# Optimization experiments

Measured on AMD Instinct MI355X. Metric: run time of the kernel, lower is better.

The kernel has to match this reference:

```python
import jax, jax.numpy as jnp
import numpy as np

HEADS = 8
DIM_HEAD = 64
SCALE = DIM_HEAD ** -0.5

def setup_inputs() -> dict:
    key = jax.random.key(0)
    ks = jax.random.split(key, 6)
    b, n, m, qd, cd = 4, 2048, 2048, 256, 256
    inner = HEADS * DIM_HEAD
    return {
        "x": jax.random.normal(ks[0], (b, n, qd), jnp.float32),
        "context": jax.random.normal(ks[1], (b, m, cd), jnp.float32),
        "Wq": jax.random.normal(ks[2], (inner, qd), jnp.float32) * 0.02,
        "bq": jnp.zeros((inner,), jnp.float32),
        "Wkv": jax.random.normal(ks[3], (2 * inner, cd), jnp.float32) * 0.02,
        "bkv": jnp.zeros((2 * inner,), jnp.float32),
        "Wo": jax.random.normal(ks[4], (qd, inner), jnp.float32) * 0.02,
        "bo": jnp.zeros((qd,), jnp.float32),
    }

def reference(x, context, Wq, bq, Wkv, bkv, Wo, bo):
    b, n, _ = x.shape
    m = context.shape[1]
    inner = HEADS * DIM_HEAD
    # 1x1 conv projections == pointwise linear
    q = jnp.einsum('bnd,ed->bne', x, Wq) + bq            # [b, n, inner]
    kv = jnp.einsum('bmd,ed->bme', context, Wkv) + bkv    # [b, m, 2*inner]
    k, v = kv[..., :inner], kv[..., inner:]
    q = q.reshape(b, n, HEADS, DIM_HEAD).transpose(0, 2, 1, 3)  # [b,h,n,d]
    k = k.reshape(b, m, HEADS, DIM_HEAD).transpose(0, 2, 1, 3)
    v = v.reshape(b, m, HEADS, DIM_HEAD).transpose(0, 2, 1, 3)
    sim = jnp.einsum('bhid,bhjd->bhij', q, k) * SCALE     # [b,h,n,m]
    attn = jax.nn.softmax(sim, axis=-1)
    out = jnp.einsum('bhij,bhjd->bhid', attn, v)          # [b,h,n,d]
    out = out.transpose(0, 2, 1, 3).reshape(b, n, inner)  # [b,n,inner]
    return jnp.einsum('bne,oe->bno', out, Wo) + bo        # [b,n,query_dim]
```

## Files before the change

### kernel.cpp

```cpp
#include <hip/hip_runtime.h>
#include <hip/hip_bf16.h>

#define NB 4
#define SEQ 2048
#define NHEADS 8

typedef __attribute__((ext_vector_type(8))) short bf16x8;
typedef __attribute__((ext_vector_type(4))) short bf16x4;
typedef __attribute__((ext_vector_type(4))) float f32x4;

__device__ inline short f2bf(float x) {
    union { float f; unsigned u; } v; v.f = x;
    unsigned r = v.u + 0x7FFF + ((v.u >> 16) & 1);
    return (short)(r >> 16);
}

__device__ inline unsigned pack2bf(float a, float b) {
    __hip_bfloat162 h = __float22bfloat162_rn(make_float2(a, b));
    unsigned u; __builtin_memcpy(&u, &h, 4);
    return u;
}

__global__ __launch_bounds__(256) void cvt_all(
    const float* __restrict__ x, const float* __restrict__ ctx,
    const float* __restrict__ wq, const float* __restrict__ wkv,
    const float* __restrict__ wo,
    short* __restrict__ xb, short* __restrict__ cb, short* __restrict__ wqb,
    short* __restrict__ wkvb, short* __restrict__ wob)
{
    const int i = blockIdx.x * 256 + threadIdx.x;
    const float* src; short* dst; int off;
    if (i < 524288)       { src = x;   dst = xb;   off = i; }
    else if (i < 1048576) { src = ctx; dst = cb;   off = i - 524288; }
    else if (i < 1081344) { src = wq;  dst = wqb;  off = i - 1048576; }
    else if (i < 1146880) { src = wkv; dst = wkvb; off = i - 1081344; }
    else                  { src = wo;  dst = wob;  off = i - 1146880; }
    const float4 v = ((const float4*)src)[off];
    uint2 o2;
    o2.x = pack2bf(v.x, v.y);
    o2.y = pack2bf(v.z, v.w);
    *(uint2*)(dst + (size_t)off * 4) = o2;
}

template <bool OUT_BF16>
__global__ __launch_bounds__(256) void gemm_bf16(
    const short* __restrict__ A,
    const short* __restrict__ W,
    const float* __restrict__ bias,
    void* __restrict__ out,
    int K, int Ccols, float scale)
{
    __shared__ short As[128 * 64];
    __shared__ short Ws[128 * 64];
    const int tid = threadIdx.x;
    const int w = tid >> 6;
    const int lane = tid & 63;
    const int low = lane & 15;
    const int quad = lane >> 4;
    const int wm = w >> 1;
    const int wn = w & 1;
    const int rM0 = blockIdx.y * 128;
    const int c0 = blockIdx.x * 128;

    const int srow = tid >> 3;
    const int sj = tid & 7;

    f32x4 acc[4][4];
#pragma unroll
    for (int mt = 0; mt < 4; ++mt)
#pragma unroll
        for (int nt = 0; nt < 4; ++nt) acc[mt][nt] = (f32x4){0.f, 0.f, 0.f, 0.f};

    bf16x8 pa[4], pwr[4];
#pragma unroll
    for (int c = 0; c < 4; ++c) {
        const int row = c * 32 + srow;
        pa[c]  = *(const bf16x8*)(A + (size_t)(rM0 + row) * K + sj * 8);
        pwr[c] = *(const bf16x8*)(W + (size_t)(c0 + row) * K + sj * 8);
    }

    int k0 = 0;
    for (;;) {
        __syncthreads();
#pragma unroll
        for (int c = 0; c < 4; ++c) {
            const int row = c * 32 + srow;
            const int pc = sj ^ (row & 7);
            *(bf16x8*)(&As[row * 64 + pc * 8]) = pa[c];
            *(bf16x8*)(&Ws[row * 64 + pc * 8]) = pwr[c];
        }
        __syncthreads();
        const int kn = k0 + 64;
        if (kn < K) {
#pragma unroll
            for (int c = 0; c < 4; ++c) {
                const int row = c * 32 + srow;
                pa[c]  = *(const bf16x8*)(A + (size_t)(rM0 + row) * K + kn + sj * 8);
                pwr[c] = *(const bf16x8*)(W + (size_t)(c0 + row) * K + kn + sj * 8);
            }
        }
#pragma unroll
        for (int kh = 0; kh < 2; ++kh) {
            bf16x8 af[4], bfv[4];
#pragma unroll
            for (int t = 0; t < 4; ++t) {
                const int ra = wm * 64 + t * 16 + low;
                af[t] = *(const bf16x8*)(&As[ra * 64 + ((kh * 4 + quad) ^ (ra & 7)) * 8]);
                const int rb = wn * 64 + t * 16 + low;
                bfv[t] = *(const bf16x8*)(&Ws[rb * 64 + ((kh * 4 + quad) ^ (rb & 7)) * 8]);
            }
#pragma unroll
            for (int mt = 0; mt < 4; ++mt)
#pragma unroll
                for (int nt = 0; nt < 4; ++nt)
                    acc[mt][nt] = __builtin_amdgcn_mfma_f32_16x16x32_bf16(af[mt], bfv[nt], acc[mt][nt], 0, 0, 0);
        }
        k0 = kn;
        if (k0 >= K) break;
    }

#pragma unroll
    for (int nt = 0; nt < 4; ++nt) {
        const int col = c0 + wn * 64 + nt * 16 + low;
        const float bv = bias[col];
#pragma unroll
        for (int mt = 0; mt < 4; ++mt) {
            const size_t rbase = (size_t)(rM0 + wm * 64 + mt * 16 + quad * 4);
#pragma unroll
            for (int r = 0; r < 4; ++r) {
                const float val = (acc[mt][nt][r] + bv) * scale;
                if (OUT_BF16) ((short*)out)[(rbase + r) * Ccols + col] = f2bf(val);
                else          ((float*)out)[(rbase + r) * Ccols + col] = val;
            }
        }
    }
}

#define KST 72
#define VST 72
#define PST 72

__global__ __launch_bounds__(256) void attn_mfma(
    const short* __restrict__ q2,
    const short* __restrict__ kv2,
    short* __restrict__ o)
{
    __shared__ short Ks[64 * KST];
    __shared__ short Vt[64 * VST];
    __shared__ short Ps[4][32 * PST];

    const int tid = threadIdx.x;
    const int w = tid >> 6;
    const int lane = tid & 63;
    const int low = lane & 15;
    const int quad = lane >> 4;

    const int bh = blockIdx.y;
    const int b = bh >> 3;
    const int h = bh & 7;
    const int iq0 = blockIdx.x * 128;

    bf16x8 qf[2][2];
#pragma unroll
    for (int qt = 0; qt < 2; ++qt)
#pragma unroll
        for (int kh = 0; kh < 2; ++kh)
            qf[qt][kh] = *(const bf16x8*)(q2 + (size_t)(b * SEQ + iq0 + w * 32 + qt * 16 + low) * 512
                                          + h * 64 + kh * 32 + quad * 8);

    const short* kbase = kv2 + (size_t)(b * SEQ) * 1024 + h * 64;
    const short* vbase = kbase + 512;
    short* pw = &Ps[w][0];

    float lsum[2][4];
#pragma unroll
    for (int qt = 0; qt < 2; ++qt)
#pragma unroll
        for (int r = 0; r < 4; ++r) lsum[qt][r] = 0.f;
    f32x4 oacc[2][4];
#pragma unroll
    for (int qt = 0; qt < 2; ++qt)
#pragma unroll
        for (int dt = 0; dt < 4; ++dt) oacc[qt][dt] = (f32x4){0.f, 0.f, 0.f, 0.f};

    const int krow = tid >> 2;
    const int kc = (tid & 3) * 16;
    const int vk4 = (tid & 15) * 4;
    const int vd4 = (tid >> 4) * 4;

    bf16x8 pk0, pk1;
    bf16x4 pv0, pv1, pv2, pv3;
    {
        const short* ksrc = kbase + (size_t)krow * 1024 + kc;
        pk0 = *(const bf16x8*)(ksrc);
        pk1 = *(const bf16x8*)(ksrc + 8);
        const short* vs = vbase + (size_t)vk4 * 1024 + vd4;
        pv0 = *(const bf16x4*)(vs);
        pv1 = *(const bf16x4*)(vs + 1024);
        pv2 = *(const bf16x4*)(vs + 2048);
        pv3 = *(const bf16x4*)(vs + 3072);
    }

    for (int jt = 0; jt < SEQ / 64; ++jt) {
        __syncthreads();
        *(bf16x8*)(&Ks[krow * KST + kc]) = pk0;
        *(bf16x8*)(&Ks[krow * KST + kc + 8]) = pk1;
        {
            bf16x4 c0_, c1_, c2_, c3_;
            c0_[0] = pv0[0]; c0_[1] = pv1[0]; c0_[2] = pv2[0]; c0_[3] = pv3[0];
            c1_[0] = pv0[1]; c1_[1] = pv1[1]; c1_[2] = pv2[1]; c1_[3] = pv3[1];
            c2_[0] = pv0[2]; c2_[1] = pv1[2]; c2_[2] = pv2[2]; c2_[3] = pv3[2];
            c3_[0] = pv0[3]; c3_[1] = pv1[3]; c3_[2] = pv2[3]; c3_[3] = pv3[3];
            *(bf16x4*)(&Vt[(vd4 + 0) * VST + vk4]) = c0_;
            *(bf16x4*)(&Vt[(vd4 + 1) * VST + vk4]) = c1_;
            *(bf16x4*)(&Vt[(vd4 + 2) * VST + vk4]) = c2_;
            *(bf16x4*)(&Vt[(vd4 + 3) * VST + vk4]) = c3_;
        }
        __syncthreads();

        if (jt + 1 < SEQ / 64) {
            const short* ksrc = kbase + (size_t)((jt + 1) * 64 + krow) * 1024 + kc;
            pk0 = *(const bf16x8*)(ksrc);
            pk1 = *(const bf16x8*)(ksrc + 8);
            const short* vs = vbase + (size_t)((jt + 1) * 64 + vk4) * 1024 + vd4;
            pv0 = *(const bf16x4*)(vs);
            pv1 = *(const bf16x4*)(vs + 1024);
            pv2 = *(const bf16x4*)(vs + 2048);
            pv3 = *(const bf16x4*)(vs + 3072);
        }

#pragma unroll
        for (int nt = 0; nt < 4; ++nt) {
            const bf16x8 kb0 = *(const bf16x8*)(&Ks[(nt * 16 + low) * KST + quad * 8]);
            const bf16x8 kb1 = *(const bf16x8*)(&Ks[(nt * 16 + low) * KST + 32 + quad * 8]);
#pragma unroll
            for (int qt = 0; qt < 2; ++qt) {
                f32x4 s = (f32x4){0.f, 0.f, 0.f, 0.f};
                s = __builtin_amdgcn_mfma_f32_16x16x32_bf16(qf[qt][0], kb0, s, 0, 0, 0);
                s = __builtin_amdgcn_mfma_f32_16x16x32_bf16(qf[qt][1], kb1, s, 0, 0, 0);
                const float p0 = __builtin_amdgcn_exp2f(s[0]);
                const float p1 = __builtin_amdgcn_exp2f(s[1]);
                const float p2 = __builtin_amdgcn_exp2f(s[2]);
                const float p3 = __builtin_amdgcn_exp2f(s[3]);
                lsum[qt][0] += p0; lsum[qt][1] += p1;
                lsum[qt][2] += p2; lsum[qt][3] += p3;
                const unsigned u01 = pack2bf(p0, p1);
                const unsigned u23 = pack2bf(p2, p3);
                short* pb = &pw[(qt * 16 + quad * 4) * PST + nt * 16 + low];
                pb[0]       = (short)(u01 & 0xffff);
                pb[PST]     = (short)(u01 >> 16);
                pb[2 * PST] = (short)(u23 & 0xffff);
                pb[3 * PST] = (short)(u23 >> 16);
            }
        }
        __builtin_amdgcn_wave_barrier();

#pragma unroll
        for (int kb = 0; kb < 2; ++kb) {
            bf16x8 pfr[2];
#pragma unroll
            for (int qt = 0; qt < 2; ++qt)
                pfr[qt] = *(const bf16x8*)(&pw[(qt * 16 + low) * PST + kb * 32 + quad * 8]);
#pragma unroll
            for (int dt = 0; dt < 4; ++dt) {
                const bf16x8 vf = *(const bf16x8*)(&Vt[(dt * 16 + low) * VST + kb * 32 + quad * 8]);
                oacc[0][dt] = __builtin_amdgcn_mfma_f32_16x16x32_bf16(pfr[0], vf, oacc[0][dt], 0, 0, 0);
                oacc[1][dt] = __builtin_amdgcn_mfma_f32_16x16x32_bf16(pfr[1], vf, oacc[1][dt], 0, 0, 0);
            }
        }
        __builtin_amdgcn_wave_barrier();
    }

#pragma unroll
    for (int qt = 0; qt < 2; ++qt) {
        float linv[4];
#pragma unroll
        for (int r = 0; r < 4; ++r) {
            float x = lsum[qt][r];
            x += __shfl_xor(x, 1);
            x += __shfl_xor(x, 2);
            x += __shfl_xor(x, 4);
            x += __shfl_xor(x, 8);
            linv[r] = 1.f / x;
        }
        short* obase = o + (size_t)(b * SEQ + iq0 + w * 32 + qt * 16 + quad * 4) * 512 + h * 64;
#pragma unroll
        for (int r = 0; r < 4; ++r)
#pragma unroll
            for (int dt = 0; dt < 4; ++dt)
                obase[(size_t)r * 512 + dt * 16 + low] = f2bf(oacc[qt][dt][r] * linv[r]);
    }
}

extern "C" void kernel_launch(void* const* d_in, const int* in_sizes, int n_in,
                              void* d_out, int out_size, void* d_ws, size_t ws_size,
                              hipStream_t stream) {
    const float* x   = (const float*)d_in[0];
    const float* ctx = (const float*)d_in[1];
    const float* Wq  = (const float*)d_in[2];
    const float* bq  = (const float*)d_in[3];
    const float* Wkv = (const float*)d_in[4];
    const float* bkv = (const float*)d_in[5];
    const float* Wo  = (const float*)d_in[6];
    const float* bo  = (const float*)d_in[7];
    float* out = (float*)d_out;

    const int ROWS = NB * SEQ;
    short* xb   = (short*)d_ws;
    short* cb   = xb + 2097152;
    short* wqb  = cb + 2097152;
    short* wkvb = wqb + 131072;
    short* wob  = wkvb + 262144;
    short* q2b  = wob + 131072;
    short* kv2b = q2b + (size_t)ROWS * 512;
    short* owsb = kv2b + (size_t)ROWS * 1024;

    cvt_all<<<4608, 256, 0, stream>>>(x, ctx, Wq, Wkv, Wo, xb, cb, wqb, wkvb, wob);

    const float qscale = 0.125f * 1.44269504088896f;
    gemm_bf16<true><<<dim3(512 / 128, ROWS / 128), 256, 0, stream>>>(
        xb, wqb, bq, q2b, 256, 512, qscale);
    gemm_bf16<true><<<dim3(1024 / 128, ROWS / 128), 256, 0, stream>>>(
        cb, wkvb, bkv, kv2b, 256, 1024, 1.0f);
    attn_mfma<<<dim3(SEQ / 128, NB * NHEADS), 256, 0, stream>>>(q2b, kv2b, owsb);
    gemm_bf16<false><<<dim3(256 / 128, ROWS / 128), 256, 0, stream>>>(
        owsb, wob, bo, out, 512, 256, 1.0f);
}
```

Measured before the change: 170.1 us.

## Fuse fp32-to-bf16 conversion into GEMMs, shrink tiles, restructure attention per wave

The separate conversion kernel is removed, and each GEMM now loads fp32 inputs and weights and packs them to bf16 while staging into shared memory. This saves one launch and a full round trip of converted activations through global memory. The Q and output projections switch to a 64x64 tile variant to get more blocks. The attention kernel now gives each wave 16 query rows instead of 32, doubling the grid, and computes S transposed (K as the A operand) so P can be written with vector stores. The trade-offs are less K/V reuse per block in attention and twice the fp32 bytes loaded in the GEMMs.

```diff
diff --git a/kernel.cpp b/kernel.cpp
--- a/kernel.cpp
+++ b/kernel.cpp
@@ -21,49 +21,28 @@
     return u;
 }
 
-__global__ __launch_bounds__(256) void cvt_all(
-    const float* __restrict__ x, const float* __restrict__ ctx,
-    const float* __restrict__ wq, const float* __restrict__ wkv,
-    const float* __restrict__ wo,
-    short* __restrict__ xb, short* __restrict__ cb, short* __restrict__ wqb,
-    short* __restrict__ wkvb, short* __restrict__ wob)
-{
-    const int i = blockIdx.x * 256 + threadIdx.x;
-    const float* src; short* dst; int off;
-    if (i < 524288)       { src = x;   dst = xb;   off = i; }
-    else if (i < 1048576) { src = ctx; dst = cb;   off = i - 524288; }
-    else if (i < 1081344) { src = wq;  dst = wqb;  off = i - 1048576; }
-    else if (i < 1146880) { src = wkv; dst = wkvb; off = i - 1081344; }
-    else                  { src = wo;  dst = wob;  off = i - 1146880; }
-    const float4 v = ((const float4*)src)[off];
-    uint2 o2;
-    o2.x = pack2bf(v.x, v.y);
-    o2.y = pack2bf(v.z, v.w);
-    *(uint2*)(dst + (size_t)off * 4) = o2;
-}
-
-template <bool OUT_BF16>
-__global__ __launch_bounds__(256) void gemm_bf16(
-    const short* __restrict__ A,
-    const short* __restrict__ W,
-    const float* __restrict__ bias,
-    void* __restrict__ out,
+__device__ inline bf16x8 pack8(float4 a, float4 b) {
+    union { unsigned u[4]; bf16x8 v; } r;
+    r.u[0] = pack2bf(a.x, a.y);
+    r.u[1] = pack2bf(a.z, a.w);
+    r.u[2] = pack2bf(b.x, b.y);
+    r.u[3] = pack2bf(b.z, b.w);
+    return r.v;
+}
+
+template <bool CVT_A, bool CVT_W, bool OUT_BF16>
+__global__ __launch_bounds__(256) void gemm128(
+    const void* __restrict__ A_, const void* __restrict__ W_,
+    const float* __restrict__ bias, void* __restrict__ out,
     int K, int Ccols, float scale)
 {
     __shared__ short As[128 * 64];
     __shared__ short Ws[128 * 64];
     const int tid = threadIdx.x;
-    const int w = tid >> 6;
-    const int lane = tid & 63;
-    const int low = lane & 15;
-    const int quad = lane >> 4;
-    const int wm = w >> 1;
-    const int wn = w & 1;
-    const int rM0 = blockIdx.y * 128;
-    const int c0 = blockIdx.x * 128;
-
-    const int srow = tid >> 3;
-    const int sj = tid & 7;
+    const int w = tid >> 6, lane = tid & 63, low = lane & 15, quad = lane >> 4;
+    const int wm = w >> 1, wn = w & 1;
+    const int rM0 = blockIdx.y * 128, c0 = blockIdx.x * 128;
+    const int srow = tid >> 3, sj = tid & 7;
 
     f32x4 acc[4][4];
 #pragma unroll
@@ -71,13 +50,32 @@
 #pragma unroll
         for (int nt = 0; nt < 4; ++nt) acc[mt][nt] = (f32x4){0.f, 0.f, 0.f, 0.f};
 
-    bf16x8 pa[4], pwr[4];
-#pragma unroll
-    for (int c = 0; c < 4; ++c) {
+    float4 paf[4][2], pwf[4][2];
+    bf16x8 pab[4], pwb[4];
+
+    auto loadA = [&](int c, int k0) {
         const int row = c * 32 + srow;
-        pa[c]  = *(const bf16x8*)(A + (size_t)(rM0 + row) * K + sj * 8);
-        pwr[c] = *(const bf16x8*)(W + (size_t)(c0 + row) * K + sj * 8);
-    }
+        if constexpr (CVT_A) {
+            const float* p = (const float*)A_ + (size_t)(rM0 + row) * K + k0 + sj * 8;
+            paf[c][0] = ((const float4*)p)[0];
+            paf[c][1] = ((const float4*)p)[1];
+        } else {
+            pab[c] = *(const bf16x8*)((const short*)A_ + (size_t)(rM0 + row) * K + k0 + sj * 8);
+        }
+    };
+    auto loadW = [&](int c, int k0) {
+        const int row = c * 32 + srow;
+        if constexpr (CVT_W) {
+            const float* p = (const float*)W_ + (size_t)(c0 + row) * K + k0 + sj * 8;
+            pwf[c][0] = ((const float4*)p)[0];
+            pwf[c][1] = ((const float4*)p)[1];
+        } else {
+            pwb[c] = *(const bf16x8*)((const short*)W_ + (size_t)(c0 + row) * K + k0 + sj * 8);
+        }
+    };
+
+#pragma unroll
+    for (int c = 0; c < 4; ++c) { loadA(c, 0); loadW(c, 0); }
 
     int k0 = 0;
     for (;;) {
@@ -86,18 +84,16 @@
         for (int c = 0; c < 4; ++c) {
             const int row = c * 32 + srow;
             const int pc = sj ^ (row & 7);
-            *(bf16x8*)(&As[row * 64 + pc * 8]) = pa[c];
-            *(bf16x8*)(&Ws[row * 64 + pc * 8]) = pwr[c];
+            if constexpr (CVT_A) *(bf16x8*)(&As[row * 64 + pc * 8]) = pack8(paf[c][0], paf[c][1]);
+            else                 *(bf16x8*)(&As[row * 64 + pc * 8]) = pab[c];
+            if constexpr (CVT_W) *(bf16x8*)(&Ws[row * 64 + pc * 8]) = pack8(pwf[c][0], pwf[c][1]);
+            else                 *(bf16x8*)(&Ws[row * 64 + pc * 8]) = pwb[c];
         }
         __syncthreads();
         const int kn = k0 + 64;
         if (kn < K) {
 #pragma unroll
-            for (int c = 0; c < 4; ++c) {
-                const int row = c * 32 + srow;
-                pa[c]  = *(const bf16x8*)(A + (size_t)(rM0 + row) * K + kn + sj * 8);
-                pwr[c] = *(const bf16x8*)(W + (size_t)(c0 + row) * K + kn + sj * 8);
-            }
+            for (int c = 0; c < 4; ++c) { loadA(c, kn); loadW(c, kn); }
         }
 #pragma unroll
         for (int kh = 0; kh < 2; ++kh) {
@@ -126,6 +122,106 @@
 #pragma unroll
         for (int mt = 0; mt < 4; ++mt) {
             const size_t rbase = (size_t)(rM0 + wm * 64 + mt * 16 + quad * 4);
+#pragma unroll
+            for (int r = 0; r < 4; ++r) {
+                const float val = (acc[mt][nt][r] + bv) * scale;
+                if (OUT_BF16) ((short*)out)[(rbase + r) * Ccols + col] = f2bf(val);
+                else          ((float*)out)[(rbase + r) * Ccols + col] = val;
+            }
+        }
+    }
+}
+
+template <bool CVT_A, bool CVT_W, bool OUT_BF16>
+__global__ __launch_bounds__(256) void gemm64(
+    const void* __restrict__ A_, const void* __restrict__ W_,
+    const float* __restrict__ bias, void* __restrict__ out,
+    int K, int Ccols, float scale)
+{
+    __shared__ short As[64 * 64];
+    __shared__ short Ws[64 * 64];
+    const int tid = threadIdx.x;
+    const int w = tid >> 6, lane = tid & 63, low = lane & 15, quad = lane >> 4;
+    const int wm = w >> 1, wn = w & 1;
+    const int r0 = blockIdx.y * 64, c0 = blockIdx.x * 64;
+    const int srow = tid >> 2;
+    const int sc = (tid & 3) * 2;
+
+    f32x4 acc[2][2];
+#pragma unroll
+    for (int mt = 0; mt < 2; ++mt)
+#pragma unroll
+        for (int nt = 0; nt < 2; ++nt) acc[mt][nt] = (f32x4){0.f, 0.f, 0.f, 0.f};
+
+    float4 paf[2][2], pwf[2][2];
+    bf16x8 pab[2], pwb[2];
+
+    auto loadA = [&](int k0) {
+        if constexpr (CVT_A) {
+            const float* p = (const float*)A_ + (size_t)(r0 + srow) * K + k0 + sc * 8;
+            paf[0][0] = ((const float4*)p)[0]; paf[0][1] = ((const float4*)p)[1];
+            paf[1][0] = ((const float4*)p)[2]; paf[1][1] = ((const float4*)p)[3];
+        } else {
+            const short* p = (const short*)A_ + (size_t)(r0 + srow) * K + k0 + sc * 8;
+            pab[0] = ((const bf16x8*)p)[0];
+            pab[1] = ((const bf16x8*)p)[1];
+        }
+    };
+    auto loadW = [&](int k0) {
+        if constexpr (CVT_W) {
+            const float* p = (const float*)W_ + (size_t)(c0 + srow) * K + k0 + sc * 8;
+            pwf[0][0] = ((const float4*)p)[0]; pwf[0][1] = ((const float4*)p)[1];
+            pwf[1][0] = ((const float4*)p)[2]; pwf[1][1] = ((const float4*)p)[3];
+        } else {
+            const short* p = (const short*)W_ + (size_t)(c0 + srow) * K + k0 + sc * 8;
+            pwb[0] = ((const bf16x8*)p)[0];
+            pwb[1] = ((const bf16x8*)p)[1];
+        }
+    };
+
+    loadA(0); loadW(0);
+
+    int k0 = 0;
+    for (;;) {
+        __syncthreads();
+#pragma unroll
+        for (int c = 0; c < 2; ++c) {
+            const int pc = (sc + c) ^ (srow & 7);
+            if constexpr (CVT_A) *(bf16x8*)(&As[srow * 64 + pc * 8]) = pack8(paf[c][0], paf[c][1]);
+            else                 *(bf16x8*)(&As[srow * 64 + pc * 8]) = pab[c];
+            if constexpr (CVT_W) *(bf16x8*)(&Ws[srow * 64 + pc * 8]) = pack8(pwf[c][0], pwf[c][1]);
+            else                 *(bf16x8*)(&Ws[srow * 64 + pc * 8]) = pwb[c];
+        }
+        __syncthreads();
+        const int kn = k0 + 64;
+        if (kn < K) { loadA(kn); loadW(kn); }
+#pragma unroll
+        for (int kh = 0; kh < 2; ++kh) {
+            bf16x8 af[2], bfv[2];
+#pragma unroll
+            for (int t = 0; t < 2; ++t) {
+                const int ra = wm * 32 + t * 16 + low;
+                af[t] = *(const bf16x8*)(&As[ra * 64 + ((kh * 4 + quad) ^ (ra & 7)) * 8]);
+                const int rb = wn * 32 + t * 16 + low;
+                bfv[t] = *(const bf16x8*)(&Ws[rb * 64 + ((kh * 4 + quad) ^ (rb & 7)) * 8]);
+            }
+#pragma unroll
+            for (int mt = 0; mt < 2; ++mt)
+#pragma unroll
+                for (int nt = 0; nt < 2; ++nt)
+                    acc[mt][nt] = __builtin_amdgcn_mfma_f32_16x16x32_bf16(af[mt], bfv[nt], acc[mt][nt], 0, 0, 0);
+        }
+        k0 = kn;
+        if (k0 >= K) break;
+    }
+
+#pragma unroll
+    for (int nt = 0; nt < 2; ++nt) {
+        const int col = c0 + wn * 32 + nt * 16 + low;
+        const float bv = bias[col];
+#pragma unroll
+        for (int mt = 0; mt < 2; ++mt) {
+            const size_t rbase = (size_t)(r0 + wm * 32 + mt * 16 + quad * 4);
 #pragma unroll
             for (int r = 0; r < 4; ++r) {
                 const float val = (acc[mt][nt][r] + bv) * scale;
@@ -147,7 +243,7 @@
 {
     __shared__ short Ks[64 * KST];
     __shared__ short Vt[64 * VST];
-    __shared__ short Ps[4][32 * PST];
+    __shared__ short Ps[4][16 * PST];
 
     const int tid = threadIdx.x;
     const int w = tid >> 6;
@@ -158,30 +254,22 @@
     const int bh = blockIdx.y;
     const int b = bh >> 3;
     const int h = bh & 7;
-    const int iq0 = blockIdx.x * 128;
-
-    bf16x8 qf[2][2];
-#pragma unroll
-    for (int qt = 0; qt < 2; ++qt)
-#pragma unroll
-        for (int kh = 0; kh < 2; ++kh)
-            qf[qt][kh] = *(const bf16x8*)(q2 + (size_t)(b * SEQ + iq0 + w * 32 + qt * 16 + low) * 512
-                                          + h * 64 + kh * 32 + quad * 8);
+    const int iq0 = blockIdx.x * 64;
+
+    bf16x8 qf[2];
+#pragma unroll
+    for (int kh = 0; kh < 2; ++kh)
+        qf[kh] = *(const bf16x8*)(q2 + (size_t)(b * SEQ + iq0 + w * 16 + low) * 512
+                                  + h * 64 + kh * 32 + quad * 8);
 
     const short* kbase = kv2 + (size_t)(b * SEQ) * 1024 + h * 64;
     const short* vbase = kbase + 512;
     short* pw = &Ps[w][0];
 
-    float lsum[2][4];
-#pragma unroll
-    for (int qt = 0; qt < 2; ++qt)
-#pragma unroll
-        for (int r = 0; r < 4; ++r) lsum[qt][r] = 0.f;
-    f32x4 oacc[2][4];
-#pragma unroll
-    for (int qt = 0; qt < 2; ++qt)
-#pragma unroll
-        for (int dt = 0; dt < 4; ++dt) oacc[qt][dt] = (f32x4){0.f, 0.f, 0.f, 0.f};
+    float lsum = 0.f;
+    f32x4 oacc[4];
+#pragma unroll
+    for (int dt = 0; dt < 4; ++dt) oacc[dt] = (f32x4){0.f, 0.f, 0.f, 0.f};
 
     const int krow = tid >> 2;
     const int kc = (tid & 3) * 16;
@@ -231,65 +319,48 @@
 
 #pragma unroll
         for (int nt = 0; nt < 4; ++nt) {
-            const bf16x8 kb0 = *(const bf16x8*)(&Ks[(nt * 16 + low) * KST + quad * 8]);
-            const bf16x8 kb1 = *(const bf16x8*)(&Ks[(nt * 16 + low) * KST + 32 + quad * 8]);
-#pragma unroll
-            for (int qt = 0; qt < 2; ++qt) {
-                f32x4 s = (f32x4){0.f, 0.f, 0.f, 0.f};
-                s = __builtin_amdgcn_mfma_f32_16x16x32_bf16(qf[qt][0], kb0, s, 0, 0, 0);
-                s = __builtin_amdgcn_mfma_f32_16x16x32_bf16(qf[qt][1], kb1, s, 0, 0, 0);
-                const float p0 = __builtin_amdgcn_exp2f(s[0]);
-                const float p1 = __builtin_amdgcn_exp2f(s[1]);
-                const float p2 = __builtin_amdgcn_exp2f(s[2]);
-                const float p3 = __builtin_amdgcn_exp2f(s[3]);
-                lsum[qt][0] += p0; lsum[qt][1] += p1;
-                lsum[qt][2] += p2; lsum[qt][3] += p3;
-                const unsigned u01 = pack2bf(p0, p1);
-                const unsigned u23 = pack2bf(p2, p3);
-                short* pb = &pw[(qt * 16 + quad * 4) * PST + nt * 16 + low];
-                pb[0]       = (short)(u01 & 0xffff);
-                pb[PST]     = (short)(u01 >> 16);
-                pb[2 * PST] = (short)(u23 & 0xffff);
-                pb[3 * PST] = (short)(u23 >> 16);
-            }
+            const bf16x8 kf0 = *(const bf16x8*)(&Ks[(nt * 16 + low) * KST + quad * 8]);
+            const bf16x8 kf1 = *(const bf16x8*)(&Ks[(nt * 16 + low) * KST + 32 + quad * 8]);
+            f32x4 s = (f32x4){0.f, 0.f, 0.f, 0.f};
+            s = __builtin_amdgcn_mfma_f32_16x16x32_bf16(kf0, qf[0], s, 0, 0, 0);
+            s = __builtin_amdgcn_mfma_f32_16x16x32_bf16(kf1, qf[1], s, 0, 0, 0);
+            const float p0 = __builtin_amdgcn_exp2f(s[0]);
+            const float p1 = __builtin_amdgcn_exp2f(s[1]);
+            const float p2 = __builtin_amdgcn_exp2f(s[2]);
+            const float p3 = __builtin_amdgcn_exp2f(s[3]);
+            lsum += (p0 + p1) + (p2 + p3);
+            uint2 u;
+            u.x = pack2bf(p0, p1);
+            u.y = pack2bf(p2, p3);
+            *(uint2*)(&pw[low * PST + nt * 16 + quad * 4]) = u;
         }
         __builtin_amdgcn_wave_barrier();
 
 #pragma unroll
         for (int kb = 0; kb < 2; ++kb) {
-            bf16x8 pfr[2];
-#pragma unroll
-            for (int qt = 0; qt < 2; ++qt)
-                pfr[qt] = *(const bf16x8*)(&pw[(qt * 16 + low) * PST + kb * 32 + quad * 8]);
+            const bf16x8 pfr = *(const bf16x8*)(&pw[low * PST + kb * 32 + quad * 8]);
 #pragma unroll
             for (int dt = 0; dt < 4; ++dt) {
                 const bf16x8 vf = *(const bf16x8*)(&Vt[(dt * 16 + low) * VST + kb * 32 + quad * 8]);
-                oacc[0][dt] = __builtin_amdgcn_mfma_f32_16x16x32_bf16(pfr[0], vf, oacc[0][dt], 0, 0, 0);
-                oacc[1][dt] = __builtin_amdgcn_mfma_f32_16x16x32_bf16(pfr[1], vf, oacc[1][dt], 0, 0, 0);
+                oacc[dt] = __builtin_amdgcn_mfma_f32_16x16x32_bf16(pfr, vf, oacc[dt], 0, 0, 0);
             }
         }
         __builtin_amdgcn_wave_barrier();
     }
 
-#pragma unroll
-    for (int qt = 0; qt < 2; ++qt) {
-        float linv[4];
-#pragma unroll
-        for (int r = 0; r < 4; ++r) {
-            float x = lsum[qt][r];
-            x += __shfl_xor(x, 1);
-            x += __shfl_xor(x, 2);
-            x += __shfl_xor(x, 4);
-            x += __shfl_xor(x, 8);
-            linv[r] = 1.f / x;
-        }
-        short* obase = o + (size_t)(b * SEQ + iq0 + w * 32 + qt * 16 + quad * 4) * 512 + h * 64;
-#pragma unroll
-        for (int r = 0; r < 4; ++r)
-#pragma unroll
-            for (int dt = 0; dt < 4; ++dt)
-                obase[(size_t)r * 512 + dt * 16 + low] = f2bf(oacc[qt][dt][r] * linv[r]);
-    }
+    lsum += __shfl_xor(lsum, 16);
+    lsum += __shfl_xor(lsum, 32);
+    float linv[4];
+#pragma unroll
+    for (int r = 0; r < 4; ++r)
+        linv[r] = 1.f / __shfl(lsum, quad * 4 + r);
+
+    short* obase = o + (size_t)(b * SEQ + iq0 + w * 16 + quad * 4) * 512 + h * 64;
+#pragma unroll
+    for (int r = 0; r < 4; ++r)
+#pragma unroll
+        for (int dt = 0; dt < 4; ++dt)
+            obase[(size_t)r * 512 + dt * 16 + low] = f2bf(oacc[dt][r] * linv[r]);
 }
 
 extern "C" void kernel_launch(void* const* d_in, const int* in_sizes, int n_in,
@@ -306,23 +377,17 @@
     float* out = (float*)d_out;
 
     const int ROWS = NB * SEQ;
-    short* xb   = (short*)d_ws;
-    short* cb   = xb + 2097152;
-    short* wqb  = cb + 2097152;
-    short* wkvb = wqb + 131072;
-    short* wob  = wkvb + 262144;
-    short* q2b  = wob + 131072;
+    short* q2b  = (short*)d_ws;
     short* kv2b = q2b + (size_t)ROWS * 512;
     short* owsb = kv2b + (size_t)ROWS * 1024;
 
-    cvt_all<<<4608, 256, 0, stream>>>(x, ctx, Wq, Wkv, Wo, xb, cb, wqb, wkvb, wob);
-
     const float qscale = 0.125f * 1.44269504088896f;
-    gemm_bf16<true><<<dim3(512 / 128, ROWS / 128), 256, 0, stream>>>(
-        xb, wqb, bq, q2b, 256, 512, qscale);
-    gemm_bf16<true><<<dim3(1024 / 128, ROWS / 128), 256, 0, stream>>>(
-        cb, wkvb, bkv, kv2b, 256, 1024, 1.0f);
-    attn_mfma<<<dim3(SEQ / 128, NB * NHEADS), 256, 0, stream>>>(q2b, kv2b, owsb);
-    gemm_bf16<false><<<dim3(256 / 128, ROWS / 128), 256, 0, stream>>>(
-        owsb, wob, bo, out, 512, 256, 1.0f);
-}
+
+    gemm64<true, true, true><<<dim3(512 / 64, ROWS / 64), 256, 0, stream>>>(
+        x, Wq, bq, q2b, 256, 512, qscale);
+    gemm128<true, true, true><<<dim3(1024 / 128, ROWS / 128), 256, 0, stream>>>(
+        ctx, Wkv, bkv, kv2b, 256, 1024, 1.0f);
+    attn_mfma<<<dim3(SEQ / 64, NB * NHEADS), 256, 0, stream>>>(q2b, kv2b, owsb);
+    gemm64<false, true, false><<<dim3(256 / 64, ROWS / 64), 256, 0, stream>>>(
+        owsb, Wo, bo, out, 512, 256, 1.0f);
+}
```

Result: slower. 193.1 us (+13.6%).
